# Performance work log

Hardware: AMD Instinct MI355X
Metric: run time of the kernel (lower is better)

## Reference

```python
import jax, jax.numpy as jnp
import numpy as np
from jax import lax

B, L, N, D, H = 32, 128, 64, 64, 4
DH = D // H


def lstm_seq(x, Wih, Whh, b, h0, c0):
    # x: [T, B, I]; PyTorch gate order i, f, g, o; bias b = b_ih + b_hh fused.
    def step(carry, xt):
        h, c = carry
        g = xt @ Wih.T + h @ Whh.T + b  # [B, 4D]
        i, f, gg, o = jnp.split(g, 4, axis=-1)
        c = jax.nn.sigmoid(f) * c + jax.nn.sigmoid(i) * jnp.tanh(gg)
        h = jax.nn.sigmoid(o) * jnp.tanh(c)
        return (h, c), h
    _, Hs = lax.scan(step, (h0, c0), x)
    return Hs  # [T, B, D]


def encode_one(x, Wih, Whh, b, pw, pb):
    # x: [T, B, 1] single variable series; per-variable LSTM encoder + temporal attn pool
    z0 = jnp.zeros((x.shape[1], Whh.shape[1]), x.dtype)
    Hs = lstm_seq(x, Wih, Whh, b, z0, z0)        # [T, B, D]
    a = jax.nn.softmax(Hs @ pw + pb, axis=0)      # softmax over time -> [T, B]
    return jnp.einsum('tb,tbd->bd', a, Hs)        # [B, D]


def decode_one(cs, Wih, Whh, b, Wh, bh, Wc, bc, ow, ob):
    # cs: [B, D]; all-zero input sequence of length L
    h0 = jnp.tanh(cs @ Wh.T + bh)
    c0 = jnp.tanh(cs @ Wc.T + bc)
    z = jnp.zeros((L, cs.shape[0], 1), cs.dtype)
    Ys = lstm_seq(z, Wih, Whh, b, h0, c0)         # [L, B, D]
    return Ys @ ow + ob                           # [L, B]


def forward(X, enc_Wih, enc_Whh, enc_b, pool_w, pool_b,
            attn_Wqkv, attn_bqkv, attn_Wo, attn_bo,
            dec_Wih, dec_Whh, dec_b, init_h_W, init_h_b, init_c_W, init_c_b,
            out_w, out_b):
    # ---- per-variable encoders (vmapped over N distinct weight sets) ----
    Xe = jnp.transpose(X[:, :L - 1, :], (2, 1, 0))[..., None]  # [N, L-1, B, 1]
    C = jax.vmap(encode_one)(Xe, enc_Wih, enc_Whh, enc_b, pool_w, pool_b)  # [N, B, D]
    C = jnp.transpose(C, (1, 0, 2))  # [B, N, D]

    # ---- cross-variable MHSA (nn.MultiheadAttention, dropout=0) ----
    qkv = C @ attn_Wqkv.T + attn_bqkv            # [B, N, 3D]
    q, k, v = jnp.split(qkv, 3, axis=-1)
    def heads(t):
        return jnp.transpose(t.reshape(B, N, H, DH), (0, 2, 1, 3))  # [B, H, N, DH]
    q, k, v = heads(q), heads(k), heads(v)
    attn = jax.nn.softmax(jnp.einsum('bhnd,bhmd->bhnm', q, k) / np.sqrt(DH), axis=-1)
    o = jnp.einsum('bhnm,bhmd->bhnd', attn, v)
    o = jnp.transpose(o, (0, 2, 1, 3)).reshape(B, N, D)
    C_star = o @ attn_Wo.T + attn_bo             # [B, N, D]

    # ---- per-variable decoders (vmapped over N) ----
    Cs = jnp.transpose(C_star, (1, 0, 2))        # [N, B, D]
    O = jax.vmap(decode_one)(Cs, dec_Wih, dec_Whh, dec_b,
                             init_h_W, init_h_b, init_c_W, init_c_b,
                             out_w, out_b)       # [N, L, B]
    recon = jnp.transpose(O[:, :L - 1, :], (2, 1, 0))  # [B, L-1, N]
    pred = O[:, L - 1, :].T                             # [B, N]
    return recon, pred, C_star


def setup_inputs() -> dict:
    key = jax.random.key(0)
    ks = jax.random.split(key, 20)
    s = 1.0 / np.sqrt(D)
    rn = lambda k, shape: (jax.random.normal(k, shape, jnp.float32) * s)
    return {
        'X': jax.random.normal(ks[0], (B, L, N), jnp.float32),
        'enc_Wih': rn(ks[1], (N, 4 * D, 1)),
        'enc_Whh': rn(ks[2], (N, 4 * D, D)),
        'enc_b': rn(ks[3], (N, 4 * D)),
        'pool_w': rn(ks[4], (N, D)),
        'pool_b': rn(ks[5], (N,)),
        'attn_Wqkv': rn(ks[6], (3 * D, D)),
        'attn_bqkv': rn(ks[7], (3 * D,)),
        'attn_Wo': rn(ks[8], (D, D)),
        'attn_bo': rn(ks[9], (D,)),
        'dec_Wih': rn(ks[10], (N, 4 * D, 1)),
        'dec_Whh': rn(ks[11], (N, 4 * D, D)),
        'dec_b': rn(ks[12], (N, 4 * D)),
        'init_h_W': rn(ks[13], (N, D, D)),
        'init_h_b': rn(ks[14], (N, D)),
        'init_c_W': rn(ks[15], (N, D, D)),
        'init_c_b': rn(ks[16], (N, D)),
        'out_w': rn(ks[17], (N, D)),
        'out_b': rn(ks[18], (N,)),
    }


def reference(X, enc_Wih, enc_Whh, enc_b, pool_w, pool_b,
              attn_Wqkv, attn_bqkv, attn_Wo, attn_bo,
              dec_Wih, dec_Whh, dec_b, init_h_W, init_h_b, init_c_W, init_c_b,
              out_w, out_b):
    return forward(X, enc_Wih, enc_Whh, enc_b, pool_w, pool_b,
                   attn_Wqkv, attn_bqkv, attn_Wo, attn_bo,
                   dec_Wih, dec_Whh, dec_b, init_h_W, init_h_b, init_c_W, init_c_b,
                   out_w, out_b)
```

## Files before the change

kernel.cpp:

```cpp
#include <hip/hip_runtime.h>
#include <cstddef>

#define BB   32
#define LL   128
#define NN   64
#define DD   64
#define HH   4

typedef float v2f __attribute__((ext_vector_type(2)));

__device__ __forceinline__ float bcast(float v, int l) {
    return __int_as_float(__builtin_amdgcn_readlane(__float_as_int(v), l));
}
__device__ __forceinline__ float sigmoidf_(float x) {
    return 1.0f / (1.0f + __expf(-x));
}
__device__ __forceinline__ float tanhf_(float x) {
    float e = __expf(2.0f * x);
    return 1.0f - 2.0f / (e + 1.0f);
}
__device__ __forceinline__ void pin(v2f& v) {
    asm volatile("" : "+v"(v));
}

#define LIST64(X) \
  X(0)  X(1)  X(2)  X(3)  X(4)  X(5)  X(6)  X(7)  \
  X(8)  X(9)  X(10) X(11) X(12) X(13) X(14) X(15) \
  X(16) X(17) X(18) X(19) X(20) X(21) X(22) X(23) \
  X(24) X(25) X(26) X(27) X(28) X(29) X(30) X(31) \
  X(32) X(33) X(34) X(35) X(36) X(37) X(38) X(39) \
  X(40) X(41) X(42) X(43) X(44) X(45) X(46) X(47) \
  X(48) X(49) X(50) X(51) X(52) X(53) X(54) X(55) \
  X(56) X(57) X(58) X(59) X(60) X(61) X(62) X(63)

#define DECLW(k) v2f wif##k, wgo##k;
#define LOADW(k) wif##k = v2f{Ri[k], Rf[k]}; wgo##k = v2f{Rg[k], Ro[k]};
#define PINW(k)  pin(wif##k); pin(wgo##k);
#define FMAK(k)  { const float hk_##k = bcast(h, k);                          \
                   const v2f hh_##k = {hk_##k, hk_##k};                       \
                   aif = __builtin_elementwise_fma(wif##k, hh_##k, aif);      \
                   ago = __builtin_elementwise_fma(wgo##k, hh_##k, ago); }

__global__ __launch_bounds__(64, 1)
void enc_kernel(const float* __restrict__ X,
                const float* __restrict__ Wih,
                const float* __restrict__ Whh,
                const float* __restrict__ bias,
                const float* __restrict__ poolw,
                const float* __restrict__ poolb,
                float* __restrict__ Cws)
{
    const int n = blockIdx.x >> 5;
    const int b = blockIdx.x & 31;
    const int u = threadIdx.x;

    const float* Ri = Whh + ((size_t)n * 256 + u) * 64;
    const float* Rf = Ri + 64 * 64;
    const float* Rg = Ri + 128 * 64;
    const float* Ro = Ri + 192 * 64;

    LIST64(DECLW)
    LIST64(LOADW)
    LIST64(PINW)

    const float* Bn = bias + n * 256;
    v2f bif = {Bn[u],       Bn[u +  64]};
    v2f bgo = {Bn[u + 128], Bn[u + 192]};
    const float* Wn = Wih + n * 256;
    v2f xif = {Wn[u],       Wn[u +  64]};
    v2f xgo = {Wn[u + 128], Wn[u + 192]};
    pin(bif); pin(bgo); pin(xif); pin(xgo);
    const float pwu = poolw[n * DD + u];
    const float pbn = poolb[n];

    const float x0 = X[(size_t)b * (LL * NN) + (size_t)u * NN + n];
    const float x1 = X[(size_t)b * (LL * NN) + (size_t)(u + 64) * NN + n];

    float h = 0.0f, c = 0.0f;
    float m = -1e30f, s = 0.0f, pa = 0.0f;

#pragma unroll 1
    for (int t = 0; t < LL - 1; ++t) {
        const float xt = bcast((t < 64) ? x0 : x1, t & 63);
        v2f aif = __builtin_elementwise_fma(xif, v2f{xt, xt}, bif);
        v2f ago = __builtin_elementwise_fma(xgo, v2f{xt, xt}, bgo);

        LIST64(FMAK)

        const float gi = sigmoidf_(aif.x), gf = sigmoidf_(aif.y);
        const float gg = tanhf_(ago.x),   go = sigmoidf_(ago.y);
        c = gf * c + gi * gg;
        h = go * tanhf_(c);

        float p = h * pwu;
#pragma unroll
        for (int off = 32; off >= 1; off >>= 1) p += __shfl_xor(p, off, 64);
        const float score = p + pbn;

        const float mn   = fmaxf(m, score);
        const float corr = __expf(m - mn);
        const float wgt  = __expf(score - mn);
        s  = s * corr + wgt;
        pa = pa * corr + wgt * h;
        m  = mn;
    }

    Cws[(size_t)b * (NN * DD) + (size_t)n * DD + u] = pa / s;
}

__global__ __launch_bounds__(256)
void attn_kernel(const float* __restrict__ Cws,
                 const float* __restrict__ Wqkv,
                 const float* __restrict__ bqkv,
                 float* __restrict__ Ows)
{
    const int b = blockIdx.x >> 2;
    const int h = blockIdx.x & 3;
    const int tid = threadIdx.x;

    __shared__ float Cl[64][65];
    __shared__ float Wl[48][65];
    __shared__ float biasl[48];
    __shared__ float ql[64][17], kl[64][17], vl[64][17];
    __shared__ float sl[64][65];

    for (int i = tid; i < 64 * 64; i += 256)
        Cl[i >> 6][i & 63] = Cws[(size_t)b * (NN * DD) + i];
    for (int i = tid; i < 48 * 64; i += 256) {
        int row = i >> 6, col = i & 63;
        int grp = row >> 4, r = row & 15;
        Wl[row][col] = Wqkv[(size_t)(grp * 64 + h * 16 + r) * DD + col];
    }
    if (tid < 48) {
        int grp = tid >> 4, r = tid & 15;
        biasl[tid] = bqkv[grp * 64 + h * 16 + r];
    }
    __syncthreads();

    for (int i = tid; i < 3 * 64 * 16; i += 256) {
        int sec = i >> 10;
        int rem = i & 1023;
        int nn = rem >> 4, dh = rem & 15;
        float acc = biasl[sec * 16 + dh];
        const float* wr = &Wl[sec * 16 + dh][0];
#pragma unroll 16
        for (int k = 0; k < 64; ++k) acc = fmaf(Cl[nn][k], wr[k], acc);
        if      (sec == 0) ql[nn][dh] = acc;
        else if (sec == 1) kl[nn][dh] = acc;
        else               vl[nn][dh] = acc;
    }
    __syncthreads();

    for (int i = tid; i < 64 * 64; i += 256) {
        int nn = i >> 6, mm = i & 63;
        float acc = 0.0f;
#pragma unroll
        for (int d = 0; d < 16; ++d) acc = fmaf(ql[nn][d], kl[mm][d], acc);
        sl[nn][mm] = acc * 0.25f;
    }
    __syncthreads();

    if (tid < 64) {
        float mx = -1e30f;
        for (int mm = 0; mm < 64; ++mm) mx = fmaxf(mx, sl[tid][mm]);
        float ss = 0.0f;
        for (int mm = 0; mm < 64; ++mm) {
            float e = __expf(sl[tid][mm] - mx);
            sl[tid][mm] = e;
            ss += e;
        }
        float inv = 1.0f / ss;
        for (int mm = 0; mm < 64; ++mm) sl[tid][mm] *= inv;
    }
    __syncthreads();

    for (int i = tid; i < 64 * 16; i += 256) {
        int nn = i >> 4, dh = i & 15;
        float acc = 0.0f;
#pragma unroll 16
        for (int mm = 0; mm < 64; ++mm) acc = fmaf(sl[nn][mm], vl[mm][dh], acc);
        Ows[(size_t)b * (NN * DD) + (size_t)nn * DD + h * 16 + dh] = acc;
    }
}

__global__ __launch_bounds__(256)
void proj_kernel(const float* __restrict__ Ows,
                 const float* __restrict__ Wo,
                 const float* __restrict__ bo,
                 float* __restrict__ Cstar)
{
    const int b = blockIdx.x;
    const int tid = threadIdx.x;
    __shared__ float Ol[64][65];
    __shared__ float Wl[64][65];

    for (int i = tid; i < 64 * 64; i += 256) {
        Ol[i >> 6][i & 63] = Ows[(size_t)b * (NN * DD) + i];
        Wl[i >> 6][i & 63] = Wo[i];
    }
    __syncthreads();

    for (int i = tid; i < 64 * 64; i += 256) {
        int nn = i >> 6, d = i & 63;
        float acc = bo[d];
#pragma unroll 16
        for (int k = 0; k < 64; ++k) acc = fmaf(Ol[nn][k], Wl[d][k], acc);
        Cstar[(size_t)b * (NN * DD) + i] = acc;
    }
}

__global__ __launch_bounds__(64)
void dec_init_kernel(const float* __restrict__ Cstar,
                     const float* __restrict__ WhI,
                     const float* __restrict__ bhI,
                     const float* __restrict__ WcI,
                     const float* __restrict__ bcI,
                     float* __restrict__ H0,
                     float* __restrict__ C0)
{
    const int n = blockIdx.x >> 5;
    const int b = blockIdx.x & 31;
    const int u = threadIdx.x;

    const float cs = Cstar[(size_t)b * (NN * DD) + (size_t)n * DD + u];
    const float4* Rh = reinterpret_cast<const float4*>(WhI + ((size_t)n * DD + u) * DD);
    const float4* Rc = reinterpret_cast<const float4*>(WcI + ((size_t)n * DD + u) * DD);
    float ah = bhI[n * DD + u];
    float ac = bcI[n * DD + u];
#pragma unroll
    for (int q = 0; q < 16; ++q) {
        const float4 wh = Rh[q], wc = Rc[q];
        float k0 = bcast(cs, 4 * q + 0);
        float k1 = bcast(cs, 4 * q + 1);
        float k2 = bcast(cs, 4 * q + 2);
        float k3 = bcast(cs, 4 * q + 3);
        ah = fmaf(wh.x, k0, ah); ah = fmaf(wh.y, k1, ah);
        ah = fmaf(wh.z, k2, ah); ah = fmaf(wh.w, k3, ah);
        ac = fmaf(wc.x, k0, ac); ac = fmaf(wc.y, k1, ac);
        ac = fmaf(wc.z, k2, ac); ac = fmaf(wc.w, k3, ac);
    }
    const size_t idx = ((size_t)n * BB + b) * DD + u;
    H0[idx] = tanhf_(ah);
    C0[idx] = tanhf_(ac);
}

__global__ __launch_bounds__(64, 1)
void dec_kernel(const float* __restrict__ Whh,
                const float* __restrict__ bias,
                const float* __restrict__ ow,
                const float* __restrict__ ob,
                const float* __restrict__ H0,
                const float* __restrict__ C0,
                float* __restrict__ recon,
                float* __restrict__ pred)
{
    const int n = blockIdx.x >> 5;
    const int b = blockIdx.x & 31;
    const int u = threadIdx.x;

    const float* Ri = Whh + ((size_t)n * 256 + u) * 64;
    const float* Rf = Ri + 64 * 64;
    const float* Rg = Ri + 128 * 64;
    const float* Ro = Ri + 192 * 64;

    LIST64(DECLW)
    LIST64(LOADW)
    LIST64(PINW)

    const float* Bn = bias + n * 256;
    v2f bif = {Bn[u],       Bn[u +  64]};
    v2f bgo = {Bn[u + 128], Bn[u + 192]};
    pin(bif); pin(bgo);
    const float owu = ow[n * DD + u];
    const float obn = ob[n];

    const size_t idx = ((size_t)n * BB + b) * DD + u;
    float h = H0[idx];
    float c = C0[idx];

#pragma unroll 1
    for (int t = 0; t < LL; ++t) {
        v2f aif = bif, ago = bgo;

        LIST64(FMAK)

        const float gi = sigmoidf_(aif.x), gf = sigmoidf_(aif.y);
        const float gg = tanhf_(ago.x),   go = sigmoidf_(ago.y);
        c = gf * c + gi * gg;
        h = go * tanhf_(c);

        float p = h * owu;
#pragma unroll
        for (int off = 32; off >= 1; off >>= 1) p += __shfl_xor(p, off, 64);
        if (u == 0) {
            const float y = p + obn;
            if (t < LL - 1)
                recon[(size_t)b * ((LL - 1) * NN) + (size_t)t * NN + n] = y;
            else
                pred[(size_t)b * NN + n] = y;
        }
    }
}

extern "C" void kernel_launch(void* const* d_in, const int* in_sizes, int n_in,
                              void* d_out, int out_size, void* d_ws, size_t ws_size,
                              hipStream_t stream) {
    (void)in_sizes; (void)n_in; (void)out_size; (void)ws_size;

    const float* X         = (const float*)d_in[0];
    const float* enc_Wih   = (const float*)d_in[1];
    const float* enc_Whh   = (const float*)d_in[2];
    const float* enc_b     = (const float*)d_in[3];
    const float* pool_w    = (const float*)d_in[4];
    const float* pool_b    = (const float*)d_in[5];
    const float* attn_Wqkv = (const float*)d_in[6];
    const float* attn_bqkv = (const float*)d_in[7];
    const float* attn_Wo   = (const float*)d_in[8];
    const float* attn_bo   = (const float*)d_in[9];
    const float* dec_Whh   = (const float*)d_in[11];
    const float* dec_b     = (const float*)d_in[12];
    const float* init_h_W  = (const float*)d_in[13];
    const float* init_h_b  = (const float*)d_in[14];
    const float* init_c_W  = (const float*)d_in[15];
    const float* init_c_b  = (const float*)d_in[16];
    const float* out_w     = (const float*)d_in[17];
    const float* out_b     = (const float*)d_in[18];

    float* out   = (float*)d_out;
    float* recon = out;
    float* pred  = out + (size_t)BB * (LL - 1) * NN;
    float* cstar = pred + (size_t)BB * NN;

    float* Cws = (float*)d_ws;
    float* Ows = Cws + (size_t)BB * NN * DD;
    float* H0 = Cws;
    float* C0 = Ows;

    enc_kernel<<<dim3(NN * BB), dim3(64), 0, stream>>>(
        X, enc_Wih, enc_Whh, enc_b, pool_w, pool_b, Cws);

    attn_kernel<<<dim3(BB * HH), dim3(256), 0, stream>>>(
        Cws, attn_Wqkv, attn_bqkv, Ows);

    proj_kernel<<<dim3(BB), dim3(256), 0, stream>>>(
        Ows, attn_Wo, attn_bo, cstar);

    dec_init_kernel<<<dim3(NN * BB), dim3(64), 0, stream>>>(
        cstar, init_h_W, init_h_b, init_c_W, init_c_b, H0, C0);

    dec_kernel<<<dim3(NN * BB), dim3(64), 0, stream>>>(
        dec_Whh, dec_b, out_w, out_b, H0, C0, recon, pred);
}
```

Baseline: 580.8 us.

## Split LSTM recurrence K-dimension across two waves sharing two batch elements

Encoder and decoder LSTM kernels now run 128-thread blocks that each handle two batch elements. Each wave holds half of the recurrent weight matrix (32 of the 64 K columns) in registers and computes partial gates for both batch elements. The partial sums and the hidden states are exchanged through shared memory with two barriers per step. This halves per-thread weight registers and the serial FMA chain per step, and halves the block count. In exchange it adds LDS traffic and synchronisation on the latency-critical recurrence.

```diff
diff --git a/kernel.cpp b/kernel.cpp
--- a/kernel.cpp
+++ b/kernel.cpp
@@ -23,25 +23,32 @@
     asm volatile("" : "+v"(v));
 }
 
-#define LIST64(X) \
-  X(0)  X(1)  X(2)  X(3)  X(4)  X(5)  X(6)  X(7)  \
-  X(8)  X(9)  X(10) X(11) X(12) X(13) X(14) X(15) \
-  X(16) X(17) X(18) X(19) X(20) X(21) X(22) X(23) \
-  X(24) X(25) X(26) X(27) X(28) X(29) X(30) X(31) \
-  X(32) X(33) X(34) X(35) X(36) X(37) X(38) X(39) \
-  X(40) X(41) X(42) X(43) X(44) X(45) X(46) X(47) \
-  X(48) X(49) X(50) X(51) X(52) X(53) X(54) X(55) \
-  X(56) X(57) X(58) X(59) X(60) X(61) X(62) X(63)
-
-#define DECLW(k) v2f wif##k, wgo##k;
-#define LOADW(k) wif##k = v2f{Ri[k], Rf[k]}; wgo##k = v2f{Rg[k], Ro[k]};
-#define PINW(k)  pin(wif##k); pin(wgo##k);
-#define FMAK(k)  { const float hk_##k = bcast(h, k);                          \
-                   const v2f hh_##k = {hk_##k, hk_##k};                       \
-                   aif = __builtin_elementwise_fma(wif##k, hh_##k, aif);      \
-                   ago = __builtin_elementwise_fma(wgo##k, hh_##k, ago); }
-
-__global__ __launch_bounds__(64, 1)
+#define KLIST(X) X(0) X(1) X(2) X(3) X(4) X(5) X(6) X(7) \
+                 X(8) X(9) X(10) X(11) X(12) X(13) X(14) X(15)
+
+#define DECLW(j) v2f wifA##j, wifB##j, wgoA##j, wgoB##j;
+#define LOADW(j) \
+    wifA##j = v2f{Ri[2*(j)],   Rf[2*(j)]};   \
+    wifB##j = v2f{Ri[2*(j)+1], Rf[2*(j)+1]}; \
+    wgoA##j = v2f{Rg[2*(j)],   Ro[2*(j)]};   \
+    wgoB##j = v2f{Rg[2*(j)+1], Ro[2*(j)+1]};
+#define PINW(j) pin(wifA##j); pin(wifB##j); pin(wgoA##j); pin(wgoB##j);
+
+#define FMAK(j) { \
+    const float ha0 = bcast(h0, kbase + 2*(j)); \
+    const float hb0 = bcast(h0, kbase + 2*(j) + 1); \
+    const float ha1 = bcast(h1, kbase + 2*(j)); \
+    const float hb1 = bcast(h1, kbase + 2*(j) + 1); \
+    aifA0 = __builtin_elementwise_fma(wifA##j, v2f{ha0,ha0}, aifA0); \
+    agoA0 = __builtin_elementwise_fma(wgoA##j, v2f{ha0,ha0}, agoA0); \
+    aifB0 = __builtin_elementwise_fma(wifB##j, v2f{hb0,hb0}, aifB0); \
+    agoB0 = __builtin_elementwise_fma(wgoB##j, v2f{hb0,hb0}, agoB0); \
+    aifA1 = __builtin_elementwise_fma(wifA##j, v2f{ha1,ha1}, aifA1); \
+    agoA1 = __builtin_elementwise_fma(wgoA##j, v2f{ha1,ha1}, agoA1); \
+    aifB1 = __builtin_elementwise_fma(wifB##j, v2f{hb1,hb1}, aifB1); \
+    agoB1 = __builtin_elementwise_fma(wgoB##j, v2f{hb1,hb1}, agoB1); }
+
+__global__ __launch_bounds__(128, 2)
 void enc_kernel(const float* __restrict__ X,
                 const float* __restrict__ Wih,
                 const float* __restrict__ Whh,
@@ -50,18 +57,25 @@
                 const float* __restrict__ poolb,
                 float* __restrict__ Cws)
 {
-    const int n = blockIdx.x >> 5;
-    const int b = blockIdx.x & 31;
-    const int u = threadIdx.x;
-
-    const float* Ri = Whh + ((size_t)n * 256 + u) * 64;
+    const int n   = blockIdx.x >> 4;
+    const int bg  = blockIdx.x & 15;
+    const int tid = threadIdx.x;
+    const int w   = tid >> 6;
+    const int u   = tid & 63;
+    const int kbase = w << 5;
+    const int bbm = 2 * bg + w;
+
+    __shared__ float4 part[2][2][64];
+    __shared__ float  hx[2][64];
+
+    const float* Ri = Whh + (size_t)n * 16384 + (size_t)u * 64 + kbase;
     const float* Rf = Ri + 64 * 64;
     const float* Rg = Ri + 128 * 64;
     const float* Ro = Ri + 192 * 64;
 
-    LIST64(DECLW)
-    LIST64(LOADW)
-    LIST64(PINW)
+    KLIST(DECLW)
+    KLIST(LOADW)
+    KLIST(PINW)
 
     const float* Bn = bias + n * 256;
     v2f bif = {Bn[u],       Bn[u +  64]};
@@ -70,42 +84,66 @@
     v2f xif = {Wn[u],       Wn[u +  64]};
     v2f xgo = {Wn[u + 128], Wn[u + 192]};
     pin(bif); pin(bgo); pin(xif); pin(xgo);
+
     const float pwu = poolw[n * DD + u];
     const float pbn = poolb[n];
 
-    const float x0 = X[(size_t)b * (LL * NN) + (size_t)u * NN + n];
-    const float x1 = X[(size_t)b * (LL * NN) + (size_t)(u + 64) * NN + n];
-
-    float h = 0.0f, c = 0.0f;
+    const float xm0 = X[(size_t)bbm * (LL * NN) + (size_t)u * NN + n];
+    const float xm1 = X[(size_t)bbm * (LL * NN) + (size_t)(u + 64) * NN + n];
+
+    float h0 = 0.0f, h1 = 0.0f, cm = 0.0f;
     float m = -1e30f, s = 0.0f, pa = 0.0f;
 
 #pragma unroll 1
     for (int t = 0; t < LL - 1; ++t) {
-        const float xt = bcast((t < 64) ? x0 : x1, t & 63);
-        v2f aif = __builtin_elementwise_fma(xif, v2f{xt, xt}, bif);
-        v2f ago = __builtin_elementwise_fma(xgo, v2f{xt, xt}, bgo);
-
-        LIST64(FMAK)
-
-        const float gi = sigmoidf_(aif.x), gf = sigmoidf_(aif.y);
-        const float gg = tanhf_(ago.x),   go = sigmoidf_(ago.y);
-        c = gf * c + gi * gg;
-        h = go * tanhf_(c);
-
-        float p = h * pwu;
+        const float xt = bcast((t < 64) ? xm0 : xm1, t & 63);
+        const v2f ini_if = __builtin_elementwise_fma(xif, v2f{xt, xt}, bif);
+        const v2f ini_go = __builtin_elementwise_fma(xgo, v2f{xt, xt}, bgo);
+        const v2f z = {0.0f, 0.0f};
+        v2f aifA0 = (w == 0) ? ini_if : z;
+        v2f agoA0 = (w == 0) ? ini_go : z;
+        v2f aifA1 = (w == 0) ? z : ini_if;
+        v2f agoA1 = (w == 0) ? z : ini_go;
+        v2f aifB0 = z, agoB0 = z, aifB1 = z, agoB1 = z;
+
+        KLIST(FMAK)
+
+        const v2f aif0 = aifA0 + aifB0, ago0 = agoA0 + agoB0;
+        const v2f aif1 = aifA1 + aifB1, ago1 = agoA1 + agoB1;
+
+        part[w][0][u] = float4{aif0.x, aif0.y, ago0.x, ago0.y};
+        part[w][1][u] = float4{aif1.x, aif1.y, ago1.x, ago1.y};
+        __syncthreads();
+        const float4 po = part[w ^ 1][w][u];
+        const v2f mine_if = (w == 0) ? aif0 : aif1;
+        const v2f mine_go = (w == 0) ? ago0 : ago1;
+        const v2f gif = mine_if + v2f{po.x, po.y};
+        const v2f ggo = mine_go + v2f{po.z, po.w};
+
+        const float gi = sigmoidf_(gif.x), gf = sigmoidf_(gif.y);
+        const float gg = tanhf_(ggo.x),    go = sigmoidf_(ggo.y);
+        cm = gf * cm + gi * gg;
+        const float hm = go * tanhf_(cm);
+
+        float p = hm * pwu;
 #pragma unroll
         for (int off = 32; off >= 1; off >>= 1) p += __shfl_xor(p, off, 64);
         const float score = p + pbn;
-
         const float mn   = fmaxf(m, score);
         const float corr = __expf(m - mn);
         const float wgt  = __expf(score - mn);
         s  = s * corr + wgt;
-        pa = pa * corr + wgt * h;
+        pa = pa * corr + wgt * hm;
         m  = mn;
-    }
-
-    Cws[(size_t)b * (NN * DD) + (size_t)n * DD + u] = pa / s;
+
+        hx[w][u] = hm;
+        __syncthreads();
+        const float ho = hx[w ^ 1][u];
+        h0 = (w == 0) ? hm : ho;
+        h1 = (w == 0) ? ho : hm;
+    }
+
+    Cws[(size_t)bbm * (NN * DD) + (size_t)n * DD + u] = pa / s;
 }
 
 __global__ __launch_bounds__(256)
@@ -244,7 +282,7 @@
     C0[idx] = tanhf_(ac);
 }
 
-__global__ __launch_bounds__(64, 1)
+__global__ __launch_bounds__(128, 2)
 void dec_kernel(const float* __restrict__ Whh,
                 const float* __restrict__ bias,
                 const float* __restrict__ ow,
@@ -254,18 +292,26 @@
                 float* __restrict__ recon,
                 float* __restrict__ pred)
 {
-    const int n = blockIdx.x >> 5;
-    const int b = blockIdx.x & 31;
-    const int u = threadIdx.x;
-
-    const float* Ri = Whh + ((size_t)n * 256 + u) * 64;
+    const int n   = blockIdx.x >> 4;
+    const int bg  = blockIdx.x & 15;
+    const int tid = threadIdx.x;
+    const int w   = tid >> 6;
+    const int u   = tid & 63;
+    const int kbase = w << 5;
+    const int bb0 = 2 * bg, bb1 = 2 * bg + 1;
+    const int bbm = 2 * bg + w;
+
+    __shared__ float4 part[2][2][64];
+    __shared__ float  hx[2][64];
+
+    const float* Ri = Whh + (size_t)n * 16384 + (size_t)u * 64 + kbase;
     const float* Rf = Ri + 64 * 64;
     const float* Rg = Ri + 128 * 64;
     const float* Ro = Ri + 192 * 64;
 
-    LIST64(DECLW)
-    LIST64(LOADW)
-    LIST64(PINW)
+    KLIST(DECLW)
+    KLIST(LOADW)
+    KLIST(PINW)
 
     const float* Bn = bias + n * 256;
     v2f bif = {Bn[u],       Bn[u +  64]};
@@ -274,31 +320,54 @@
     const float owu = ow[n * DD + u];
     const float obn = ob[n];
 
-    const size_t idx = ((size_t)n * BB + b) * DD + u;
-    float h = H0[idx];
-    float c = C0[idx];
+    float h0 = H0[((size_t)n * BB + bb0) * DD + u];
+    float h1 = H0[((size_t)n * BB + bb1) * DD + u];
+    float cm = C0[((size_t)n * BB + bbm) * DD + u];
 
 #pragma unroll 1
     for (int t = 0; t < LL; ++t) {
-        v2f aif = bif, ago = bgo;
-
-        LIST64(FMAK)
-
-        const float gi = sigmoidf_(aif.x), gf = sigmoidf_(aif.y);
-        const float gg = tanhf_(ago.x),   go = sigmoidf_(ago.y);
-        c = gf * c + gi * gg;
-        h = go * tanhf_(c);
-
-        float p = h * owu;
+        const v2f z = {0.0f, 0.0f};
+        v2f aifA0 = (w == 0) ? bif : z;
+        v2f agoA0 = (w == 0) ? bgo : z;
+        v2f aifA1 = (w == 0) ? z : bif;
+        v2f agoA1 = (w == 0) ? z : bgo;
+        v2f aifB0 = z, agoB0 = z, aifB1 = z, agoB1 = z;
+
+        KLIST(FMAK)
+
+        const v2f aif0 = aifA0 + aifB0, ago0 = agoA0 + agoB0;
+        const v2f aif1 = aifA1 + aifB1, ago1 = agoA1 + agoB1;
+
+        part[w][0][u] = float4{aif0.x, aif0.y, ago0.x, ago0.y};
+        part[w][1][u] = float4{aif1.x, aif1.y, ago1.x, ago1.y};
+        __syncthreads();
+        const float4 po = part[w ^ 1][w][u];
+        const v2f mine_if = (w == 0) ? aif0 : aif1;
+        const v2f mine_go = (w == 0) ? ago0 : ago1;
+        const v2f gif = mine_if + v2f{po.x, po.y};
+        const v2f ggo = mine_go + v2f{po.z, po.w};
+
+        const float gi = sigmoidf_(gif.x), gf = sigmoidf_(gif.y);
+        const float gg = tanhf_(ggo.x),    go = sigmoidf_(ggo.y);
+        cm = gf * cm + gi * gg;
+        const float hm = go * tanhf_(cm);
+
+        float p = hm * owu;
 #pragma unroll
         for (int off = 32; off >= 1; off >>= 1) p += __shfl_xor(p, off, 64);
         if (u == 0) {
             const float y = p + obn;
             if (t < LL - 1)
-                recon[(size_t)b * ((LL - 1) * NN) + (size_t)t * NN + n] = y;
+                recon[(size_t)bbm * ((LL - 1) * NN) + (size_t)t * NN + n] = y;
             else
-                pred[(size_t)b * NN + n] = y;
+                pred[(size_t)bbm * NN + n] = y;
         }
+
+        hx[w][u] = hm;
+        __syncthreads();
+        const float ho = hx[w ^ 1][u];
+        h0 = (w == 0) ? hm : ho;
+        h1 = (w == 0) ? ho : hm;
     }
 }
 
@@ -336,7 +405,7 @@
     float* H0 = Cws;
     float* C0 = Ows;
 
-    enc_kernel<<<dim3(NN * BB), dim3(64), 0, stream>>>(
+    enc_kernel<<<dim3(NN * 16), dim3(128), 0, stream>>>(
         X, enc_Wih, enc_Whh, enc_b, pool_w, pool_b, Cws);
 
     attn_kernel<<<dim3(BB * HH), dim3(256), 0, stream>>>(
@@ -348,6 +417,6 @@
     dec_init_kernel<<<dim3(NN * BB), dim3(64), 0, stream>>>(
         cstar, init_h_W, init_h_b, init_c_W, init_c_b, H0, C0);
 
-    dec_kernel<<<dim3(NN * BB), dim3(64), 0, stream>>>(
+    dec_kernel<<<dim3(NN * 16), dim3(128), 0, stream>>>(
         dec_Whh, dec_b, out_w, out_b, H0, C0, recon, pred);
 }
```

New measurement: 528.4 us. 9.0% less time.
